# Kernel optimization log

Hardware: AMD Instinct MI355X
Metric: run time of the kernel (lower is better)

## Reference

```python
import jax, jax.numpy as jnp
import numpy as np

N = 10000
C = 16
AVG_DEG = 32
TAU = 1.0


def _label_propagate(adj, labels, train_mask, gumbel, iter_step, k_hop):
    # Faithful port of ContextLabel.LabelPropagate + get_label_distribution.
    m = train_mask[:, None]  # [N,1] bool
    Y = jnp.where(m, labels, jnp.zeros_like(labels))  # Y_pred init: zeros w/ train rows set
    for _ in range(iter_step):
        Y = adj @ Y                      # [N,N]@[N,C] propagation (memory-bound, C small)
        Y = jnp.where(m, labels, Y)      # masked overwrite of train rows
    if k_hop == 0:
        return Y
    # F.gumbel_softmax(Y, hard=True), tau=1: straight-through one-hot
    logits = (Y + gumbel) / TAU
    soft = jax.nn.softmax(logits, axis=-1)
    hard = jax.nn.one_hot(jnp.argmax(logits, axis=-1), C, dtype=soft.dtype)
    Y = hard + soft - jax.lax.stop_gradient(soft)
    Y = jnp.where(m, labels, Y)
    # k-hop adjacency power (loop over static k_hop-1)
    a = adj
    for _ in range(k_hop - 1):
        a = a @ adj
    # get_label_distribution: torch builds a dense [N,N,C] tensor with labels[j] at every
    # nonzero (i,j) of a, then sums over dim=1. That is exactly (a != 0).float() @ labels,
    # with no gradient through the nonzero pattern — computed without the N*N*C intermediate.
    mask = jax.lax.stop_gradient((a != 0).astype(Y.dtype))
    dist = mask @ Y  # [N,C] sum of neighbor label vectors
    dist = dist / jnp.sum(dist, axis=1, keepdims=True)
    return dist


def _make_adj(key):
    k1, k2 = jax.random.split(key)
    pattern = jax.random.uniform(k1, (N, N)) < (AVG_DEG / N)  # ~32 neighbors/row
    vals = jax.random.uniform(k2, (N, N))
    a = jnp.where(pattern, vals, 0.0).astype(jnp.float32)
    a = a.at[jnp.arange(N), jnp.arange(N)].set(1.0)  # self-loops -> no empty rows
    return a / jnp.sum(a, axis=1, keepdims=True)     # row-normalized


def setup_inputs() -> dict:
    key = jax.random.key(0)
    ka, kn, kl, km, kg1, kg2 = jax.random.split(key, 6)
    adj = _make_adj(ka)             # the (perturbed) adjacency passed to forward
    adj_norm = _make_adj(kn)        # the fixed adjacency used in __init__
    labels_int = jax.random.randint(kl, (N,), 0, C)
    labels_onehot = jax.nn.one_hot(labels_int, C, dtype=jnp.float32)
    train_mask = jax.random.uniform(km, (N,)) < 0.1
    # gumbel noise: -log(-log(U)), U clipped away from {0,1}
    def gum(k):
        u = jax.random.uniform(k, (N, C), minval=1e-6, maxval=1.0 - 1e-6)
        return -jnp.log(-jnp.log(u))
    gumbel_init = gum(kg1)
    gumbel = gum(kg2)
    # pseudo_labels = detached LabelPropagate(adj_norm, labels_onehot) from __init__
    pseudo_labels = _label_propagate(adj_norm, labels_onehot, train_mask, gumbel_init,
                                     iter_step=10, k_hop=1)
    return {"adj": adj, "labels_onehot": labels_onehot, "pseudo_labels": pseudo_labels,
            "gumbel": gumbel, "train_mask": train_mask, "iter_step": 10, "k_hop": 1}


def reference(adj, labels_onehot, pseudo_labels, gumbel, train_mask, iter_step, k_hop):
    out = _label_propagate(adj, labels_onehot, train_mask, gumbel, iter_step, k_hop)
    return jnp.mean((out - pseudo_labels) ** 2)  # F.mse_loss(..., reduction='mean')
```

## Files before the change

kernel.cpp:

```cpp
#include <hip/hip_runtime.h>

#define NN 10000
#define CC 16
#define CAP 96
#define NBLK 625

__device__ __forceinline__ bool mask_at(const void* p, int i, int mode) {
    if (mode == 0) return ((const int*)p)[i] != 0;
    if (mode == 1) return ((const unsigned char*)p)[i] != 0;
    return ((const float*)p)[i] != 0.0f;
}

__global__ __launch_bounds__(256) void build_csr(const float* __restrict__ adj,
                                                 int2* __restrict__ pack,
                                                 int* __restrict__ cnt,
                                                 const unsigned int* __restrict__ mask_words,
                                                 int* __restrict__ flag,
                                                 unsigned int* __restrict__ done) {
    if (blockIdx.x == NN) {
        __shared__ int s_int_bad, s_flt_bad;
        if (threadIdx.x == 0) { s_int_bad = 0; s_flt_bad = 0; *done = 0u; }
        __syncthreads();
        for (int i = threadIdx.x; i < NN / 4; i += 256) {
            unsigned w = mask_words[i];
            if (w > 1u) s_int_bad = 1;
            if (w != 0u && w != 0x3F800000u) s_flt_bad = 1;
        }
        __syncthreads();
        if (threadIdx.x == 0) {
            int mode;
            if (!s_int_bad)      mode = 0;
            else if (!s_flt_bad) mode = 2;
            else                 mode = 1;
            *flag = mode;
        }
        return;
    }
    __shared__ int lcnt;
    const int row = blockIdx.x;
    if (threadIdx.x == 0) lcnt = 0;
    __syncthreads();
    const float4* rp = (const float4*)(adj + (size_t)row * NN);
    int2* pb = pack + row * CAP;
    for (int i = threadIdx.x; i < NN / 4; i += 256) {
        float4 v = rp[i];
        int j = i * 4;
        if (v.x != 0.f) { int p = atomicAdd(&lcnt, 1); if (p < CAP) pb[p] = make_int2(j,     __float_as_int(v.x)); }
        if (v.y != 0.f) { int p = atomicAdd(&lcnt, 1); if (p < CAP) pb[p] = make_int2(j + 1, __float_as_int(v.y)); }
        if (v.z != 0.f) { int p = atomicAdd(&lcnt, 1); if (p < CAP) pb[p] = make_int2(j + 2, __float_as_int(v.z)); }
        if (v.w != 0.f) { int p = atomicAdd(&lcnt, 1); if (p < CAP) pb[p] = make_int2(j + 3, __float_as_int(v.w)); }
    }
    __syncthreads();
    if (threadIdx.x == 0) cnt[row] = (lcnt < CAP) ? lcnt : CAP;
}

__global__ __launch_bounds__(256) void spmv_first(const int2* __restrict__ pack,
                                                  const int* __restrict__ cnt,
                                                  const float* __restrict__ labels,
                                                  const void* __restrict__ tmask,
                                                  const int* __restrict__ flag,
                                                  float* __restrict__ Yout) {
    int t = blockIdx.x * 256 + threadIdx.x;
    int row = t >> 4, c = t & 15;
    int n = cnt[row];
    int mode = *flag;
    const int2* pp = pack + row * CAP;
    float acc = 0.0f;
    #pragma unroll 4
    for (int k = 0; k < n; k++) {
        int2 e = pp[k];
        float yv = mask_at(tmask, e.x, mode) ? labels[e.x * CC + c] : 0.0f;
        acc = fmaf(__int_as_float(e.y), yv, acc);
    }
    bool m = mask_at(tmask, row, mode);
    Yout[t] = m ? labels[t] : acc;
}

__global__ __launch_bounds__(256) void spmv_step(const int2* __restrict__ pack,
                                                 const int* __restrict__ cnt,
                                                 const float* __restrict__ Yin,
                                                 const float* __restrict__ labels,
                                                 const void* __restrict__ tmask,
                                                 const int* __restrict__ flag,
                                                 float* __restrict__ Yout) {
    int t = blockIdx.x * 256 + threadIdx.x;
    int row = t >> 4, c = t & 15;
    int n = cnt[row];
    const int2* pp = pack + row * CAP;
    float acc = 0.0f;
    #pragma unroll 4
    for (int k = 0; k < n; k++) {
        int2 e = pp[k];
        acc = fmaf(__int_as_float(e.y), Yin[e.x * CC + c], acc);
    }
    bool m = mask_at(tmask, row, *flag);
    Yout[t] = m ? labels[t] : acc;
}

__global__ __launch_bounds__(256) void spmv_harden(const int2* __restrict__ pack,
                                                   const int* __restrict__ cnt,
                                                   const float* __restrict__ Yin,
                                                   const float* __restrict__ labels,
                                                   const float* __restrict__ gumbel,
                                                   const void* __restrict__ tmask,
                                                   const int* __restrict__ flag,
                                                   float* __restrict__ Yout) {
    int t = blockIdx.x * 256 + threadIdx.x;
    int row = t >> 4, c = t & 15;
    int n = cnt[row];
    const int2* pp = pack + row * CAP;
    float acc = 0.0f;
    #pragma unroll 4
    for (int k = 0; k < n; k++) {
        int2 e = pp[k];
        acc = fmaf(__int_as_float(e.y), Yin[e.x * CC + c], acc);
    }
    bool m = mask_at(tmask, row, *flag);
    float lbl = labels[t];
    float y10 = m ? lbl : acc;
    float l = y10 + gumbel[t];
    float mx = l;
    for (int off = 8; off >= 1; off >>= 1) mx = fmaxf(mx, __shfl_xor(mx, off, 16));
    float e = expf(l - mx);
    float s = e;
    for (int off = 8; off >= 1; off >>= 1) s += __shfl_xor(s, off, 16);
    float soft = e / s;
    float hard = (l == mx) ? 1.0f : 0.0f;
    float y = (hard + soft) - soft;
    Yout[t] = m ? lbl : y;
}

__global__ __launch_bounds__(256) void mask_spmv_loss(const int2* __restrict__ pack,
                                                      const int* __restrict__ cnt,
                                                      const float* __restrict__ Y2,
                                                      const float* __restrict__ pseudo,
                                                      float* __restrict__ partial,
                                                      unsigned int* __restrict__ done,
                                                      float* __restrict__ out) {
    int t = blockIdx.x * 256 + threadIdx.x;
    int row = t >> 4, c = t & 15;
    int n = cnt[row];
    const int2* pp = pack + row * CAP;
    float acc = 0.0f;
    #pragma unroll 4
    for (int k = 0; k < n; k++) acc += Y2[pp[k].x * CC + c];
    float rs = acc;
    for (int off = 8; off >= 1; off >>= 1) rs += __shfl_xor(rs, off, 16);
    float d = acc / rs - pseudo[t];
    float contrib = d * d * (1.0f / (NN * CC));
    for (int off = 32; off >= 1; off >>= 1) contrib += __shfl_down(contrib, off, 64);
    __shared__ float sw[4];
    __shared__ int s_last;
    if ((threadIdx.x & 63) == 0) sw[threadIdx.x >> 6] = contrib;
    __syncthreads();
    if (threadIdx.x == 0) {
        partial[blockIdx.x] = sw[0] + sw[1] + sw[2] + sw[3];
        __threadfence();
        unsigned prev = __hip_atomic_fetch_add(done, 1u, __ATOMIC_ACQ_REL,
                                               __HIP_MEMORY_SCOPE_AGENT);
        s_last = (prev == NBLK - 1);
    }
    __syncthreads();
    if (!s_last) return;
    float s = 0.0f;
    for (int i = threadIdx.x; i < NBLK; i += 256)
        s += __hip_atomic_load(&partial[i], __ATOMIC_RELAXED, __HIP_MEMORY_SCOPE_AGENT);
    for (int off = 32; off >= 1; off >>= 1) s += __shfl_down(s, off, 64);
    if ((threadIdx.x & 63) == 0) sw[threadIdx.x >> 6] = s;
    __syncthreads();
    if (threadIdx.x == 0) out[0] = sw[0] + sw[1] + sw[2] + sw[3];
}

extern "C" void kernel_launch(void* const* d_in, const int* in_sizes, int n_in,
                              void* d_out, int out_size, void* d_ws, size_t ws_size,
                              hipStream_t stream) {
    const float* adj    = (const float*)d_in[0];
    const float* labels = (const float*)d_in[1];
    const float* pseudo = (const float*)d_in[2];
    const float* gumbel = (const float*)d_in[3];
    const void*  tmask  = d_in[4];

    char* ws = (char*)d_ws;
    int*          flag    = (int*)(ws + 0);
    unsigned int* done    = (unsigned int*)(ws + 8);
    int*          cnt     = (int*)(ws + 64);
    int2*         pack    = (int2*)(ws + 40064);
    float*        Ya      = (float*)(ws + 7720064);
    float*        Yb      = (float*)(ws + 8360064);
    float*        partial = (float*)(ws + 9000064);

    float* outp = (float*)d_out;

    build_csr<<<NN + 1, 256, 0, stream>>>(adj, pack, cnt, (const unsigned int*)tmask,
                                          flag, done);

    spmv_first<<<NBLK, 256, 0, stream>>>(pack, cnt, labels, tmask, flag, Ya);
    float* cur = Ya;
    float* nxt = Yb;
    for (int it = 0; it < 8; ++it) {
        spmv_step<<<NBLK, 256, 0, stream>>>(pack, cnt, cur, labels, tmask, flag, nxt);
        float* tmp = cur; cur = nxt; nxt = tmp;
    }
    spmv_harden<<<NBLK, 256, 0, stream>>>(pack, cnt, cur, labels, gumbel, tmask, flag, nxt);
    mask_spmv_loss<<<NBLK, 256, 0, stream>>>(pack, cnt, nxt, pseudo, partial, done, outp);
}
```

Before: 647.7 us.

## Fuse SpMV chain into one persistent kernel with software grid barriers

Replaces the eleven separate SpMV, harden and loss kernel launches with a single persistent kernel of 625 blocks. Iterations are separated by a custom grid barrier built from per-block generation slots, with block 0 gathering arrivals and publishing a release flag. The aim is to remove per-launch overhead and drain gaps between dependent iterations. In exchange it depends on all 625 blocks being co-resident, which the launch bounds of 4 blocks per CU are meant to ensure; otherwise the kernel could deadlock, and the barrier adds spin-wait latency.

After: 1.553 ms. 140% more time.

```diff
diff --git a/kernel.cpp b/kernel.cpp
--- a/kernel.cpp
+++ b/kernel.cpp
@@ -16,10 +16,13 @@
                                                  int* __restrict__ cnt,
                                                  const unsigned int* __restrict__ mask_words,
                                                  int* __restrict__ flag,
-                                                 unsigned int* __restrict__ done) {
+                                                 unsigned int* __restrict__ slots,
+                                                 unsigned int* __restrict__ rel) {
     if (blockIdx.x == NN) {
+        for (int i = threadIdx.x; i < NBLK; i += 256) slots[i] = 0u;
+        if (threadIdx.x == 0) *rel = 0u;
         __shared__ int s_int_bad, s_flt_bad;
-        if (threadIdx.x == 0) { s_int_bad = 0; s_flt_bad = 0; *done = 0u; }
+        if (threadIdx.x == 0) { s_int_bad = 0; s_flt_bad = 0; }
         __syncthreads();
         for (int i = threadIdx.x; i < NN / 4; i += 256) {
             unsigned w = mask_words[i];
@@ -54,17 +57,64 @@
     if (threadIdx.x == 0) cnt[row] = (lcnt < CAP) ? lcnt : CAP;
 }
 
-__global__ __launch_bounds__(256) void spmv_first(const int2* __restrict__ pack,
-                                                  const int* __restrict__ cnt,
-                                                  const float* __restrict__ labels,
-                                                  const void* __restrict__ tmask,
-                                                  const int* __restrict__ flag,
-                                                  float* __restrict__ Yout) {
-    int t = blockIdx.x * 256 + threadIdx.x;
-    int row = t >> 4, c = t & 15;
-    int n = cnt[row];
-    int mode = *flag;
+__device__ __forceinline__ void grid_barrier(int bid, unsigned gen,
+                                             unsigned* slots, unsigned* rel) {
+    __syncthreads();
+    if (threadIdx.x == 0)
+        __hip_atomic_store(&slots[bid], gen, __ATOMIC_RELEASE, __HIP_MEMORY_SCOPE_AGENT);
+    if (bid == 0) {
+        for (;;) {
+            int ok = 1;
+            for (int i = threadIdx.x; i < NBLK; i += 256) {
+                unsigned v = __hip_atomic_load(&slots[i], __ATOMIC_ACQUIRE,
+                                               __HIP_MEMORY_SCOPE_AGENT);
+                if (v < gen) ok = 0;
+            }
+            if (__syncthreads_and(ok)) break;
+            __builtin_amdgcn_s_sleep(2);
+        }
+        if (threadIdx.x == 0)
+            __hip_atomic_store(rel, gen, __ATOMIC_RELEASE, __HIP_MEMORY_SCOPE_AGENT);
+        __syncthreads();
+    } else {
+        if (threadIdx.x == 0) {
+            while (__hip_atomic_load(rel, __ATOMIC_ACQUIRE,
+                                     __HIP_MEMORY_SCOPE_AGENT) < gen)
+                __builtin_amdgcn_s_sleep(8);
+        }
+        __syncthreads();
+    }
+}
+
+__device__ __forceinline__ float spmv_row(const int2* __restrict__ pp, int n,
+                                          const float* __restrict__ Yin, int c) {
+    float acc = 0.0f;
+    #pragma unroll 4
+    for (int k = 0; k < n; k++) {
+        int2 e = pp[k];
+        acc = fmaf(__int_as_float(e.y), Yin[e.x * CC + c], acc);
+    }
+    return acc;
+}
+
+__global__ __launch_bounds__(256, 4) void mega_chain(
+        const int2* __restrict__ pack, const int* __restrict__ cnt,
+        const float* __restrict__ labels, const float* __restrict__ pseudo,
+        const float* __restrict__ gumbel, const void* __restrict__ tmask,
+        const int* __restrict__ flag,
+        unsigned* __restrict__ slots, unsigned* __restrict__ rel,
+        float* __restrict__ Ya, float* __restrict__ Yb,
+        float* __restrict__ partial, float* __restrict__ out) {
+    const int bid = blockIdx.x;
+    const int t = bid * 256 + threadIdx.x;
+    const int row = t >> 4, c = t & 15;
+    const int n = cnt[row];
     const int2* pp = pack + row * CAP;
+    const int mode = *flag;
+    const bool m = mask_at(tmask, row, mode);
+    const float lbl = labels[t];
+    unsigned gen = 0;
+
     float acc = 0.0f;
     #pragma unroll 4
     for (int k = 0; k < n; k++) {
@@ -72,52 +122,20 @@
         float yv = mask_at(tmask, e.x, mode) ? labels[e.x * CC + c] : 0.0f;
         acc = fmaf(__int_as_float(e.y), yv, acc);
     }
-    bool m = mask_at(tmask, row, mode);
-    Yout[t] = m ? labels[t] : acc;
-}
-
-__global__ __launch_bounds__(256) void spmv_step(const int2* __restrict__ pack,
-                                                 const int* __restrict__ cnt,
-                                                 const float* __restrict__ Yin,
-                                                 const float* __restrict__ labels,
-                                                 const void* __restrict__ tmask,
-                                                 const int* __restrict__ flag,
-                                                 float* __restrict__ Yout) {
-    int t = blockIdx.x * 256 + threadIdx.x;
-    int row = t >> 4, c = t & 15;
-    int n = cnt[row];
-    const int2* pp = pack + row * CAP;
-    float acc = 0.0f;
-    #pragma unroll 4
-    for (int k = 0; k < n; k++) {
-        int2 e = pp[k];
-        acc = fmaf(__int_as_float(e.y), Yin[e.x * CC + c], acc);
-    }
-    bool m = mask_at(tmask, row, *flag);
-    Yout[t] = m ? labels[t] : acc;
-}
-
-__global__ __launch_bounds__(256) void spmv_harden(const int2* __restrict__ pack,
-                                                   const int* __restrict__ cnt,
-                                                   const float* __restrict__ Yin,
-                                                   const float* __restrict__ labels,
-                                                   const float* __restrict__ gumbel,
-                                                   const void* __restrict__ tmask,
-                                                   const int* __restrict__ flag,
-                                                   float* __restrict__ Yout) {
-    int t = blockIdx.x * 256 + threadIdx.x;
-    int row = t >> 4, c = t & 15;
-    int n = cnt[row];
-    const int2* pp = pack + row * CAP;
-    float acc = 0.0f;
-    #pragma unroll 4
-    for (int k = 0; k < n; k++) {
-        int2 e = pp[k];
-        acc = fmaf(__int_as_float(e.y), Yin[e.x * CC + c], acc);
-    }
-    bool m = mask_at(tmask, row, *flag);
-    float lbl = labels[t];
-    float y10 = m ? lbl : acc;
+    float* cur = Ya;
+    float* nxt = Yb;
+    cur[t] = m ? lbl : acc;
+    grid_barrier(bid, ++gen, slots, rel);
+
+    for (int it = 0; it < 8; ++it) {
+        float a = spmv_row(pp, n, cur, c);
+        nxt[t] = m ? lbl : a;
+        float* tmp = cur; cur = nxt; nxt = tmp;
+        grid_barrier(bid, ++gen, slots, rel);
+    }
+
+    float a10 = spmv_row(pp, n, cur, c);
+    float y10 = m ? lbl : a10;
     float l = y10 + gumbel[t];
     float mx = l;
     for (int off = 8; off >= 1; off >>= 1) mx = fmaxf(mx, __shfl_xor(mx, off, 16));
@@ -127,48 +145,33 @@
     float soft = e / s;
     float hard = (l == mx) ? 1.0f : 0.0f;
     float y = (hard + soft) - soft;
-    Yout[t] = m ? lbl : y;
-}
-
-__global__ __launch_bounds__(256) void mask_spmv_loss(const int2* __restrict__ pack,
-                                                      const int* __restrict__ cnt,
-                                                      const float* __restrict__ Y2,
-                                                      const float* __restrict__ pseudo,
-                                                      float* __restrict__ partial,
-                                                      unsigned int* __restrict__ done,
-                                                      float* __restrict__ out) {
-    int t = blockIdx.x * 256 + threadIdx.x;
-    int row = t >> 4, c = t & 15;
-    int n = cnt[row];
-    const int2* pp = pack + row * CAP;
-    float acc = 0.0f;
+    nxt[t] = m ? lbl : y;
+    const float* Y2 = nxt;
+    grid_barrier(bid, ++gen, slots, rel);
+
+    float acc2 = 0.0f;
     #pragma unroll 4
-    for (int k = 0; k < n; k++) acc += Y2[pp[k].x * CC + c];
-    float rs = acc;
+    for (int k = 0; k < n; k++) acc2 += Y2[pp[k].x * CC + c];
+    float rs = acc2;
     for (int off = 8; off >= 1; off >>= 1) rs += __shfl_xor(rs, off, 16);
-    float d = acc / rs - pseudo[t];
+    float d = acc2 / rs - pseudo[t];
     float contrib = d * d * (1.0f / (NN * CC));
     for (int off = 32; off >= 1; off >>= 1) contrib += __shfl_down(contrib, off, 64);
     __shared__ float sw[4];
-    __shared__ int s_last;
     if ((threadIdx.x & 63) == 0) sw[threadIdx.x >> 6] = contrib;
     __syncthreads();
-    if (threadIdx.x == 0) {
-        partial[blockIdx.x] = sw[0] + sw[1] + sw[2] + sw[3];
-        __threadfence();
-        unsigned prev = __hip_atomic_fetch_add(done, 1u, __ATOMIC_ACQ_REL,
-                                               __HIP_MEMORY_SCOPE_AGENT);
-        s_last = (prev == NBLK - 1);
-    }
-    __syncthreads();
-    if (!s_last) return;
-    float s = 0.0f;
-    for (int i = threadIdx.x; i < NBLK; i += 256)
-        s += __hip_atomic_load(&partial[i], __ATOMIC_RELAXED, __HIP_MEMORY_SCOPE_AGENT);
-    for (int off = 32; off >= 1; off >>= 1) s += __shfl_down(s, off, 64);
-    if ((threadIdx.x & 63) == 0) sw[threadIdx.x >> 6] = s;
-    __syncthreads();
-    if (threadIdx.x == 0) out[0] = sw[0] + sw[1] + sw[2] + sw[3];
+    if (threadIdx.x == 0) partial[bid] = sw[0] + sw[1] + sw[2] + sw[3];
+    grid_barrier(bid, ++gen, slots, rel);
+
+    if (bid == 0) {
+        float ss = 0.0f;
+        for (int i = threadIdx.x; i < NBLK; i += 256)
+            ss += __hip_atomic_load(&partial[i], __ATOMIC_RELAXED, __HIP_MEMORY_SCOPE_AGENT);
+        for (int off = 32; off >= 1; off >>= 1) ss += __shfl_down(ss, off, 64);
+        if ((threadIdx.x & 63) == 0) sw[threadIdx.x >> 6] = ss;
+        __syncthreads();
+        if (threadIdx.x == 0) out[0] = sw[0] + sw[1] + sw[2] + sw[3];
+    }
 }
 
 extern "C" void kernel_launch(void* const* d_in, const int* in_sizes, int n_in,
@@ -182,25 +185,18 @@
 
     char* ws = (char*)d_ws;
     int*          flag    = (int*)(ws + 0);
-    unsigned int* done    = (unsigned int*)(ws + 8);
-    int*          cnt     = (int*)(ws + 64);
-    int2*         pack    = (int2*)(ws + 40064);
-    float*        Ya      = (float*)(ws + 7720064);
-    float*        Yb      = (float*)(ws + 8360064);
-    float*        partial = (float*)(ws + 9000064);
+    unsigned int* rel     = (unsigned int*)(ws + 4);
+    unsigned int* slots   = (unsigned int*)(ws + 64);
+    int*          cnt     = (int*)(ws + 2624);
+    int2*         pack    = (int2*)(ws + 42624);
+    float*        Ya      = (float*)(ws + 7722624);
+    float*        Yb      = (float*)(ws + 8362624);
+    float*        partial = (float*)(ws + 9002624);
 
     float* outp = (float*)d_out;
 
     build_csr<<<NN + 1, 256, 0, stream>>>(adj, pack, cnt, (const unsigned int*)tmask,
-                                          flag, done);
-
-    spmv_first<<<NBLK, 256, 0, stream>>>(pack, cnt, labels, tmask, flag, Ya);
-    float* cur = Ya;
-    float* nxt = Yb;
-    for (int it = 0; it < 8; ++it) {
-        spmv_step<<<NBLK, 256, 0, stream>>>(pack, cnt, cur, labels, tmask, flag, nxt);
-        float* tmp = cur; cur = nxt; nxt = tmp;
-    }
-    spmv_harden<<<NBLK, 256, 0, stream>>>(pack, cnt, cur, labels, gumbel, tmask, flag, nxt);
-    mask_spmv_loss<<<NBLK, 256, 0, stream>>>(pack, cnt, nxt, pseudo, partial, done, outp);
-}
+                                          flag, slots, rel);
+    mega_chain<<<NBLK, 256, 0, stream>>>(pack, cnt, labels, pseudo, gumbel, tmask,
+                                         flag, slots, rel, Ya, Yb, partial, outp);
+}
```
